# Kernel optimization log

Measured on AMD Instinct MI355X. Metric: run time of the kernel, lower is better.

The kernel has to match this reference:

```python
import jax, jax.numpy as jnp
import numpy as np

BS, N, T, D, R = 64, 256, 32, 512, 8
DK = D // R  # 64 == key_feature_dim


def setup_inputs() -> dict:
    key = jax.random.key(0)
    ks = jax.random.split(key, 20)
    s = 0.02
    p = lambda k, shape: jax.random.normal(k, shape, jnp.float32) * s
    return {
        "v": jax.random.normal(ks[0], (BS, N, D), jnp.float32),
        "b": jax.random.normal(ks[1], (BS, N, D), jnp.float32),
        "v_mask": jnp.ones((BS, N), jnp.float32),
        "t": jax.random.normal(ks[2], (BS, T, D), jnp.float32),
        "t_mask": jnp.ones((BS, T), jnp.float32),
        "WG1_w": p(ks[3], (D, D)), "WG1_b": p(ks[4], (D,)),
        "WG2_w": p(ks[5], (D, D)), "WG2_b": p(ks[6], (D,)),
        "WK_w": p(ks[7], (D, D)), "WK_b": p(ks[8], (D,)),
        "WQ_w": p(ks[9], (D, D)), "WQ_b": p(ks[10], (D,)),
        "WV_w": p(ks[11], (D, D)), "WV_b": p(ks[12], (D,)),
        "tc_w": p(ks[13], (D, 1)), "tc_b": p(ks[14], (1,)),
        "tmap_w": p(ks[15], (D, N * N)), "tmap_b": p(ks[16], (N * N,)),
    }


def _forward(v, b, v_mask, t, t_mask,
             WG1_w, WG1_b, WG2_w, WG2_b, WK_w, WK_b, WQ_w, WQ_b, WV_w, WV_b,
             tc_w, tc_b, tmap_w, tmap_b):
    bs, num_obj, dim = v.shape
    n_rel = R
    dk = dim // n_rel  # dim_per_rel == dim_k

    def shape4(x):  # (bs, N, D) -> (bs, R, N, dk)
        return x.reshape(bs, num_obj, n_rel, dk).transpose(0, 2, 1, 3)

    # --- text summary branch ---
    t_m = t * t_mask[:, :, None]                       # (bs, T, D)
    tc = t_m @ tc_w + tc_b                             # (bs, T, 1)
    tc = jnp.where(t_mask[:, :, None] == 0, -jnp.inf, tc)
    t_sscore = jax.nn.sigmoid(tc)                      # sigmoid(-inf) = 0 for pad
    t_summary = jnp.einsum('btd,bt->bd', t_m, t_sscore[..., 0])   # (bs, D)
    tmap = jax.nn.relu(t_summary @ tmap_w + tmap_b)
    tmap = tmap.reshape(bs, 1, num_obj, num_obj)       # broadcast over relations

    # --- geometric pairwise score ---
    wg1 = shape4((b @ WG1_w + WG1_b) * v_mask[:, :, None])
    wg2 = shape4((b @ WG2_w + WG2_b) * v_mask[:, :, None])
    w_g = jax.nn.relu(jnp.einsum('brnd,brmd->brnm', wg1, wg2)) + tmap

    # --- scaled dot-product score ---
    wk = shape4(v @ WK_w + WK_b)
    wq = shape4(v @ WQ_w + WQ_b)
    scaled_dot = jnp.einsum('brnd,brmd->brnm', wk, wq) / jnp.sqrt(jnp.float32(dk))

    # --- combine, mask, softmax, weighted sum ---
    w_mn = jnp.log(jnp.maximum(w_g, 1e-6)) + scaled_dot
    w_mn = jnp.where((v_mask == 0)[:, None, None, :], -jnp.inf, w_mn)
    attn = jax.nn.softmax(w_mn, axis=-1)               # (bs, R, N, N)

    wv = shape4(v @ WV_w + WV_b)
    out = jnp.einsum('brnm,brmd->brnd', attn, wv)
    out = out.transpose(0, 2, 1, 3).reshape(bs, num_obj, dim)
    return out + v


def reference(v, b, v_mask, t, t_mask,
              WG1_w, WG1_b, WG2_w, WG2_b, WK_w, WK_b, WQ_w, WQ_b, WV_w, WV_b,
              tc_w, tc_b, tmap_w, tmap_b):
    return _forward(v, b, v_mask, t, t_mask,
                    WG1_w, WG1_b, WG2_w, WG2_b, WK_w, WK_b, WQ_w, WQ_b,
                    WV_w, WV_b, tc_w, tc_b, tmap_w, tmap_b)
```

## Files before the change

kernel.cpp:

```cpp
#include <hip/hip_runtime.h>
#include <math.h>

#define BS 64
#define NOBJ 256
#define TTOK 32
#define DIM 512
#define NREL 8
#define DKK 64
#define NN 65536

typedef __attribute__((ext_vector_type(8))) short bf16x8;
typedef __attribute__((ext_vector_type(4))) float f32x4;

__device__ __forceinline__ unsigned short f2bf(float x) {
    union { float f; unsigned int u; } c; c.f = x;
    unsigned int u = c.u;
    return (unsigned short)((u + 0x7fffu + ((u >> 16) & 1u)) >> 16);
}
__device__ __forceinline__ float bf2f(unsigned short h) {
    union { unsigned int u; float f; } c; c.u = ((unsigned int)h) << 16;
    return c.f;
}
__device__ __forceinline__ void gl2lds16(const unsigned short* g, unsigned short* l) {
    __builtin_amdgcn_global_load_lds((const __attribute__((address_space(1))) void*)g,
                                     (__attribute__((address_space(3))) void*)l, 16, 0, 0);
}

__global__ void k_text(const float* __restrict__ tt, const float* __restrict__ t_mask,
                       const float* __restrict__ tc_w, const float* __restrict__ tc_b,
                       unsigned short* __restrict__ ts_bf) {
    int b = blockIdx.x;
    int tid = threadIdx.x;
    __shared__ float red[TTOK][8];
    __shared__ float sc[TTOK];
    {
        int tok = tid >> 3, seg = tid & 7;
        const float* tp = tt + (size_t)(b * TTOK + tok) * DIM + seg * 64;
        const float* wp = tc_w + seg * 64;
        float s = 0.f;
#pragma unroll
        for (int i = 0; i < 16; ++i) {
            float4 a = *(const float4*)(tp + i * 4);
            float4 w = *(const float4*)(wp + i * 4);
            s += a.x * w.x + a.y * w.y + a.z * w.z + a.w * w.w;
        }
        red[tok][seg] = s;
    }
    __syncthreads();
    if (tid < TTOK) {
        float s = 0.f;
#pragma unroll
        for (int i = 0; i < 8; ++i) s += red[tid][i];
        float m = t_mask[b * TTOK + tid];
        float tc = m * s + tc_b[0];
        float sig = 1.f / (1.f + __expf(-tc));
        sc[tid] = (m != 0.f) ? m * sig : 0.f;
    }
    __syncthreads();
    for (int d = tid; d < DIM; d += 256) {
        float acc = 0.f;
#pragma unroll
        for (int tok = 0; tok < TTOK; ++tok)
            acc += tt[(size_t)(b * TTOK + tok) * DIM + d] * sc[tok];
        ts_bf[b * DIM + d] = f2bf(acc);
    }
}

__global__ void k_convert(const float* __restrict__ v, const float* __restrict__ b,
                          unsigned short* __restrict__ v_bf, unsigned short* __restrict__ b_bf) {
    const float* src = blockIdx.y ? b : v;
    unsigned short* dst = blockIdx.y ? b_bf : v_bf;
    size_t i = ((size_t)blockIdx.x * 256 + threadIdx.x) * 4;
    float4 a = *(const float4*)(src + i);
    ushort4 o;
    o.x = f2bf(a.x); o.y = f2bf(a.y); o.z = f2bf(a.z); o.w = f2bf(a.w);
    *(ushort4*)(dst + i) = o;
}

__global__ void k_wt(const float* __restrict__ w0, const float* __restrict__ w1,
                     const float* __restrict__ w2, const float* __restrict__ w3,
                     const float* __restrict__ w4, unsigned short* __restrict__ WT) {
    int wsel = blockIdx.z;
    const float* W = wsel == 0 ? w0 : wsel == 1 ? w1 : wsel == 2 ? w2 : wsel == 3 ? w3 : w4;
    int k0 = blockIdx.x * 64, d0 = blockIdx.y * 64;
    __shared__ float tile[64][65];
    int tid = threadIdx.x;
#pragma unroll
    for (int p = 0; p < 16; ++p) {
        int lin = p * 256 + tid;
        int kk = lin >> 6, dd = lin & 63;
        tile[kk][dd] = W[(size_t)(k0 + kk) * DIM + d0 + dd];
    }
    __syncthreads();
    unsigned short* outp = WT + (size_t)wsel * DIM * DIM;
#pragma unroll
    for (int p = 0; p < 16; ++p) {
        int lin = p * 256 + tid;
        int dd = lin >> 6, kk = lin & 63;
        outp[(size_t)(d0 + dd) * DIM + k0 + kk] = f2bf(tile[kk][dd]);
    }
}

__launch_bounds__(256)
__global__ void k_tmap(const unsigned short* __restrict__ ts_bf,
                       const float* __restrict__ tmap_w, const float* __restrict__ tmap_b,
                       unsigned short* __restrict__ tmap) {
    int j0 = blockIdx.x * 64;
    int tid = threadIdx.x;
    int w = tid >> 6, lane = tid & 63, q = lane >> 4, li = lane & 15;
    __shared__ __align__(16) unsigned short Bt[64][40];
    f32x4 acc[4];
#pragma unroll
    for (int ct = 0; ct < 4; ++ct) acc[ct] = (f32x4){0.f, 0.f, 0.f, 0.f};

    for (int ks = 0; ks < 16; ++ks) {
        int k0 = ks * 32;
#pragma unroll
        for (int p = 0; p < 8; ++p) {
            int kk = (tid >> 6) + p * 4;
            int c = tid & 63;
            Bt[c][kk] = f2bf(tmap_w[(size_t)(k0 + kk) * NN + j0 + c]);
        }
        __syncthreads();
        bf16x8 a = *(const bf16x8*)(ts_bf + (size_t)(w * 16 + li) * DIM + k0 + q * 8);
#pragma unroll
        for (int ct = 0; ct < 4; ++ct) {
            bf16x8 bb = *(const bf16x8*)(&Bt[ct * 16 + li][q * 8]);
            acc[ct] = __builtin_amdgcn_mfma_f32_16x16x32_bf16(a, bb, acc[ct], 0, 0, 0);
        }
        __syncthreads();
    }
#pragma unroll
    for (int ct = 0; ct < 4; ++ct) {
        int j = j0 + ct * 16 + li;
        float bias = tmap_b[j];
#pragma unroll
        for (int i = 0; i < 4; ++i) {
            int bb = w * 16 + q * 4 + i;
            float val = fmaxf(acc[ct][i] + bias, 0.f);
            tmap[(size_t)bb * NN + j] = f2bf(val);
        }
    }
}

__launch_bounds__(256)
__global__ void k_proj(const unsigned short* __restrict__ v_bf, const unsigned short* __restrict__ b_bf,
                       const unsigned short* __restrict__ WT,
                       const float* __restrict__ bias0, const float* __restrict__ bias1,
                       const float* __restrict__ bias2, const float* __restrict__ bias3,
                       const float* __restrict__ bias4, const float* __restrict__ v_mask,
                       unsigned short* __restrict__ wg1, unsigned short* __restrict__ wg2,
                       unsigned short* __restrict__ wk, unsigned short* __restrict__ wq,
                       unsigned short* __restrict__ wvT) {
    int bx = blockIdx.x;
    int by = blockIdx.y;
    int m0 = bx * 128;
    int wsel = by >> 2;
    const unsigned short* A = (wsel < 2) ? b_bf : v_bf;
    int tid = threadIdx.x;
    int w = tid >> 6, lane = tid & 63, q = lane >> 4, li = lane & 15;
    int rh = w & 1, ch = w >> 1;

    __shared__ __align__(16) unsigned short smem[128 * 136];
    unsigned short* As = smem;
    unsigned short* Bs = smem + 4096;

    f32x4 acc[4][4];
#pragma unroll
    for (int rt = 0; rt < 4; ++rt)
#pragma unroll
        for (int ct = 0; ct < 4; ++ct) acc[rt][ct] = (f32x4){0.f, 0.f, 0.f, 0.f};

    const unsigned short* WTb = WT + (size_t)by * 128 * DIM;

    int rho = lane >> 2;
    int qs = (lane & 3) ^ ((lane >> 3) & 3);
    int rA0 = w * 16 + rho, rA1 = (w + 4) * 16 + rho;
    const unsigned short* Ag0 = A + (size_t)(m0 + rA0) * DIM + qs * 8;
    const unsigned short* Ag1 = A + (size_t)(m0 + rA1) * DIM + qs * 8;
    const unsigned short* Bg0 = WTb + (size_t)rA0 * DIM + qs * 8;
    const unsigned short* Bg1 = WTb + (size_t)rA1 * DIM + qs * 8;
    unsigned short* Al0 = As + w * 512;
    unsigned short* Al1 = As + (w + 4) * 512;
    unsigned short* Bl0 = Bs + w * 512;
    unsigned short* Bl1 = Bs + (w + 4) * 512;

    int sseg = (q ^ ((li >> 1) & 3)) * 8;

    for (int ks = 0; ks < 16; ++ks) {
        int k0 = ks * 32;
        gl2lds16(Ag0 + k0, Al0);
        gl2lds16(Ag1 + k0, Al1);
        gl2lds16(Bg0 + k0, Bl0);
        gl2lds16(Bg1 + k0, Bl1);
        __syncthreads();
        bf16x8 af[4], bfr[4];
#pragma unroll
        for (int rt = 0; rt < 4; ++rt)
            af[rt] = *(const bf16x8*)(As + (rh * 64 + rt * 16 + li) * 32 + sseg);
#pragma unroll
        for (int ct = 0; ct < 4; ++ct)
            bfr[ct] = *(const bf16x8*)(Bs + (ch * 64 + ct * 16 + li) * 32 + sseg);
#pragma unroll
        for (int rt = 0; rt < 4; ++rt)
#pragma unroll
            for (int ct = 0; ct < 4; ++ct)
                acc[rt][ct] = __builtin_amdgcn_mfma_f32_16x16x32_bf16(af[rt], bfr[ct], acc[rt][ct], 0, 0, 0);
        __syncthreads();
    }

    const float* bias = wsel == 0 ? bias0 : wsel == 1 ? bias1 : wsel == 2 ? bias2 : wsel == 3 ? bias3 : bias4;
    int dblk = (by & 3) * 128;

    if (wsel < 4) {
#pragma unroll
        for (int ct = 0; ct < 4; ++ct) {
            int d = dblk + ch * 64 + ct * 16 + li;
            float bs = bias[d];
#pragma unroll
            for (int rt = 0; rt < 4; ++rt) {
#pragma unroll
                for (int i = 0; i < 4; ++i) {
                    int bn = m0 + rh * 64 + rt * 16 + q * 4 + i;
                    float val = acc[rt][ct][i] + bs;
                    if (wsel < 2) val *= v_mask[bn];
                    unsigned short h = f2bf(val);
                    if (wsel == 0)      wg1[(size_t)bn * DIM + d] = h;
                    else if (wsel == 1) wg2[(size_t)bn * DIM + d] = h;
                    else if (wsel == 2) wk[(size_t)bn * DIM + d] = h;
                    else                wq[(size_t)bn * DIM + d] = h;
                }
            }
        }
    } else {
        unsigned short (*T)[136] = (unsigned short (*)[136])smem;
#pragma unroll
        for (int ct = 0; ct < 4; ++ct) {
            int d_local = ch * 64 + ct * 16 + li;
            float bs = bias[dblk + d_local];
#pragma unroll
            for (int rt = 0; rt < 4; ++rt) {
#pragma unroll
                for (int i = 0; i < 4; ++i) {
                    int n_local = rh * 64 + rt * 16 + q * 4 + i;
                    T[d_local][n_local] = f2bf(acc[rt][ct][i] + bs);
                }
            }
        }
        __syncthreads();
        int b = m0 >> 8, nbase = m0 & 255;
        int dl = tid >> 1;
        int nh = (tid & 1) * 64;
        int d = dblk + dl;
        int rr = d >> 6, dk = d & 63;
        unsigned short* dst = wvT + ((size_t)(b * NREL + rr) * DKK + dk) * NOBJ + nbase + nh;
#pragma unroll
        for (int k = 0; k < 8; ++k)
            *(bf16x8*)(dst + k * 8) = *(const bf16x8*)(&T[dl][nh + k * 8]);
    }
}

__launch_bounds__(256)
__global__ void k_attn(const unsigned short* __restrict__ wg1, const unsigned short* __restrict__ wg2,
                       const unsigned short* __restrict__ wk, const unsigned short* __restrict__ wq,
                       const unsigned short* __restrict__ wvT,
                       const unsigned short* __restrict__ tmap, const float* __restrict__ v_mask,
                       const float* __restrict__ v, float* __restrict__ out) {
    int br = blockIdx.x;
    int nt = blockIdx.y;
    int b = br >> 3, r = br & 7;
    int n0 = nt * 32;
    int tid = threadIdx.x;
    int w = tid >> 6, lane = tid & 63, q = lane >> 4, li = lane & 15;
    int rt = w & 1, ch = w >> 1;

    __shared__ __align__(16) unsigned short P_lds[32][264];
    __shared__ float redmax[2][32];
    __shared__ float redsum[2][32];
    __shared__ float linv[32];

    bf16x8 ag[2], ak[2];
    {
        int n = n0 + rt * 16 + li;
        const unsigned short* g1p = wg1 + (size_t)(b * NOBJ + n) * DIM + r * DKK;
        const unsigned short* kp  = wk  + (size_t)(b * NOBJ + n) * DIM + r * DKK;
#pragma unroll
        for (int ks = 0; ks < 2; ++ks) {
            ag[ks] = *(const bf16x8*)(g1p + ks * 32 + q * 8);
            ak[ks] = *(const bf16x8*)(kp + ks * 32 + q * 8);
        }
    }

    float sreg[32];
    float mloc[4] = {-INFINITY, -INFINITY, -INFINITY, -INFINITY};
#pragma unroll
    for (int j8 = 0; j8 < 8; ++j8) {
        int j = ch * 8 + j8;
        int mcol = j * 16 + li;
        const unsigned short* g2p = wg2 + (size_t)(b * NOBJ + mcol) * DIM + r * DKK;
        const unsigned short* qp  = wq  + (size_t)(b * NOBJ + mcol) * DIM + r * DKK;
        f32x4 accG = (f32x4){0.f, 0.f, 0.f, 0.f};
        f32x4 accK = (f32x4){0.f, 0.f, 0.f, 0.f};
#pragma unroll
        for (int ks = 0; ks < 2; ++ks) {
            bf16x8 bg = *(const bf16x8*)(g2p + ks * 32 + q * 8);
            accG = __builtin_amdgcn_mfma_f32_16x16x32_bf16(ag[ks], bg, accG, 0, 0, 0);
            bf16x8 bq = *(const bf16x8*)(qp + ks * 32 + q * 8);
            accK = __builtin_amdgcn_mfma_f32_16x16x32_bf16(ak[ks], bq, accK, 0, 0, 0);
        }
        float vm = v_mask[b * NOBJ + mcol];
#pragma unroll
        for (int i = 0; i < 4; ++i) {
            int n = n0 + rt * 16 + q * 4 + i;
            float tm = bf2f(tmap[(size_t)b * NN + n * 256 + mcol]);
            float g = fmaxf(accG[i], 0.f) + tm;
            float s = __logf(fmaxf(g, 1e-6f)) + accK[i] * 0.125f;
            if (vm == 0.f) s = -INFINITY;
            sreg[j8 * 4 + i] = s;
            mloc[i] = fmaxf(mloc[i], s);
        }
    }
#pragma unroll
    for (int i = 0; i < 4; ++i) {
        float m = mloc[i];
        m = fmaxf(m, __shfl_xor(m, 1));
        m = fmaxf(m, __shfl_xor(m, 2));
        m = fmaxf(m, __shfl_xor(m, 4));
        m = fmaxf(m, __shfl_xor(m, 8));
        mloc[i] = m;
    }
    if (li == 0) {
#pragma unroll
        for (int i = 0; i < 4; ++i) redmax[ch][rt * 16 + q * 4 + i] = mloc[i];
    }
    __syncthreads();
    float rowM[4], sloc[4];
#pragma unroll
    for (int i = 0; i < 4; ++i) {
        int row = rt * 16 + q * 4 + i;
        rowM[i] = fmaxf(redmax[0][row], redmax[1][row]);
        sloc[i] = 0.f;
    }
#pragma unroll
    for (int j8 = 0; j8 < 8; ++j8) {
        int j = ch * 8 + j8;
#pragma unroll
        for (int i = 0; i < 4; ++i) {
            float p = __expf(sreg[j8 * 4 + i] - rowM[i]);
            sloc[i] += p;
            P_lds[rt * 16 + q * 4 + i][j * 16 + li] = f2bf(p);
        }
    }
#pragma unroll
    for (int i = 0; i < 4; ++i) {
        float s = sloc[i];
        s += __shfl_xor(s, 1);
        s += __shfl_xor(s, 2);
        s += __shfl_xor(s, 4);
        s += __shfl_xor(s, 8);
        sloc[i] = s;
    }
    if (li == 0) {
#pragma unroll
        for (int i = 0; i < 4; ++i) redsum[ch][rt * 16 + q * 4 + i] = sloc[i];
    }
    __syncthreads();
    if (tid < 32) linv[tid] = 1.f / (redsum[0][tid] + redsum[1][tid]);
    __syncthreads();

    f32x4 o[2];
    o[0] = (f32x4){0.f, 0.f, 0.f, 0.f};
    o[1] = (f32x4){0.f, 0.f, 0.f, 0.f};
#pragma unroll
    for (int ks = 0; ks < 8; ++ks) {
        bf16x8 a = *(const bf16x8*)(&P_lds[rt * 16 + li][ks * 32 + q * 8]);
#pragma unroll
        for (int c2 = 0; c2 < 2; ++c2) {
            int dkc = (ch * 2 + c2) * 16 + li;
            bf16x8 bb = *(const bf16x8*)(wvT + (size_t)(br * DKK + dkc) * NOBJ + ks * 32 + q * 8);
            o[c2] = __builtin_amdgcn_mfma_f32_16x16x32_bf16(a, bb, o[c2], 0, 0, 0);
        }
    }
#pragma unroll
    for (int c2 = 0; c2 < 2; ++c2) {
        int dkc = (ch * 2 + c2) * 16 + li;
        int d = r * DKK + dkc;
#pragma unroll
        for (int i = 0; i < 4; ++i) {
            int row = rt * 16 + q * 4 + i;
            int n = n0 + row;
            size_t idx = (size_t)(b * NOBJ + n) * DIM + d;
            out[idx] = o[c2][i] * linv[row] + v[idx];
        }
    }
}

extern "C" void kernel_launch(void* const* d_in, const int* in_sizes, int n_in,
                              void* d_out, int out_size, void* d_ws, size_t ws_size,
                              hipStream_t stream) {
    const float* v      = (const float*)d_in[0];
    const float* b      = (const float*)d_in[1];
    const float* v_mask = (const float*)d_in[2];
    const float* t      = (const float*)d_in[3];
    const float* t_mask = (const float*)d_in[4];
    const float* WG1_w  = (const float*)d_in[5];
    const float* WG1_b  = (const float*)d_in[6];
    const float* WG2_w  = (const float*)d_in[7];
    const float* WG2_b  = (const float*)d_in[8];
    const float* WK_w   = (const float*)d_in[9];
    const float* WK_b   = (const float*)d_in[10];
    const float* WQ_w   = (const float*)d_in[11];
    const float* WQ_b   = (const float*)d_in[12];
    const float* WV_w   = (const float*)d_in[13];
    const float* WV_b   = (const float*)d_in[14];
    const float* tc_w   = (const float*)d_in[15];
    const float* tc_b   = (const float*)d_in[16];
    const float* tmap_w = (const float*)d_in[17];
    const float* tmap_b = (const float*)d_in[18];
    float* out = (float*)d_out;

    char* ws = (char*)d_ws;
    size_t off = 0;
    auto alloc = [&](size_t bytes) {
        void* p = ws + off;
        off += (bytes + 255) & ~(size_t)255;
        return p;
    };
    unsigned short* ts_bf = (unsigned short*)alloc((size_t)BS * DIM * 2);
    unsigned short* tmap  = (unsigned short*)alloc((size_t)BS * NN * 2);
    unsigned short* v_bf  = (unsigned short*)alloc((size_t)BS * NOBJ * DIM * 2);
    unsigned short* b_bf  = (unsigned short*)alloc((size_t)BS * NOBJ * DIM * 2);
    unsigned short* WT    = (unsigned short*)alloc((size_t)5 * DIM * DIM * 2);
    unsigned short* wg1   = (unsigned short*)alloc((size_t)BS * NOBJ * DIM * 2);
    unsigned short* wg2   = (unsigned short*)alloc((size_t)BS * NOBJ * DIM * 2);
    unsigned short* wk    = (unsigned short*)alloc((size_t)BS * NOBJ * DIM * 2);
    unsigned short* wq    = (unsigned short*)alloc((size_t)BS * NOBJ * DIM * 2);
    unsigned short* wvT   = (unsigned short*)alloc((size_t)BS * NOBJ * DIM * 2);

    k_text<<<dim3(BS), dim3(256), 0, stream>>>(t, t_mask, tc_w, tc_b, ts_bf);
    k_convert<<<dim3(8192, 2), dim3(256), 0, stream>>>(v, b, v_bf, b_bf);
    k_wt<<<dim3(8, 8, 5), dim3(256), 0, stream>>>(WG1_w, WG2_w, WK_w, WQ_w, WV_w, WT);
    k_tmap<<<dim3(1024), dim3(256), 0, stream>>>(ts_bf, tmap_w, tmap_b, tmap);
    k_proj<<<dim3(128, 20), dim3(256), 0, stream>>>(v_bf, b_bf, WT,
                                                    WG1_b, WG2_b, WK_b, WQ_b, WV_b, v_mask,
                                                    wg1, wg2, wk, wq, wvT);
    k_attn<<<dim3(512, 8), dim3(256), 0, stream>>>(wg1, wg2, wk, wq, wvT, tmap, v_mask, v, out);
}
```

Measured before the change: 499.8 us.

## Restructure attention into per-wave online softmax and single-wave tmap GEMM

The attention kernel now runs one block per (batch, relation). Each wave owns 64 query rows and streams key columns in chunks of 32 with an online-softmax (flash-style) accumulator, so the cross-wave LDS reductions and block barriers go away. The tmap GEMM is rewritten as a 64-thread block that loads the weights straight from global into registers and reuses each B fragment across four row tiles, with no LDS staging or syncs. The trade-off is much higher register pressure (large accumulator arrays) and only 512 attention blocks, which could hurt occupancy. The tmap kernel also does strided scalar global loads of the weights.

```diff
diff --git a/kernel.cpp b/kernel.cpp
--- a/kernel.cpp
+++ b/kernel.cpp
@@ -101,44 +101,49 @@
     }
 }
 
-__launch_bounds__(256)
+__launch_bounds__(64)
 __global__ void k_tmap(const unsigned short* __restrict__ ts_bf,
                        const float* __restrict__ tmap_w, const float* __restrict__ tmap_b,
                        unsigned short* __restrict__ tmap) {
-    int j0 = blockIdx.x * 64;
-    int tid = threadIdx.x;
-    int w = tid >> 6, lane = tid & 63, q = lane >> 4, li = lane & 15;
-    __shared__ __align__(16) unsigned short Bt[64][40];
-    f32x4 acc[4];
-#pragma unroll
-    for (int ct = 0; ct < 4; ++ct) acc[ct] = (f32x4){0.f, 0.f, 0.f, 0.f};
-
-    for (int ks = 0; ks < 16; ++ks) {
-        int k0 = ks * 32;
-#pragma unroll
-        for (int p = 0; p < 8; ++p) {
-            int kk = (tid >> 6) + p * 4;
-            int c = tid & 63;
-            Bt[c][kk] = f2bf(tmap_w[(size_t)(k0 + kk) * NN + j0 + c]);
-        }
-        __syncthreads();
-        bf16x8 a = *(const bf16x8*)(ts_bf + (size_t)(w * 16 + li) * DIM + k0 + q * 8);
+    int col0 = blockIdx.x * 64;
+    int lane = threadIdx.x;
+    int q = lane >> 4, li = lane & 15;
+    f32x4 acc[4][4];
+#pragma unroll
+    for (int rt = 0; rt < 4; ++rt)
+#pragma unroll
+        for (int ct = 0; ct < 4; ++ct) acc[rt][ct] = (f32x4){0.f, 0.f, 0.f, 0.f};
+
+    for (int kt = 0; kt < 16; ++kt) {
+        int k0 = kt * 32;
+        bf16x8 a[4];
+#pragma unroll
+        for (int rt = 0; rt < 4; ++rt)
+            a[rt] = *(const bf16x8*)(ts_bf + (size_t)(rt * 16 + li) * DIM + k0 + q * 8);
 #pragma unroll
         for (int ct = 0; ct < 4; ++ct) {
-            bf16x8 bb = *(const bf16x8*)(&Bt[ct * 16 + li][q * 8]);
-            acc[ct] = __builtin_amdgcn_mfma_f32_16x16x32_bf16(a, bb, acc[ct], 0, 0, 0);
-        }
-        __syncthreads();
+            const float* wp = tmap_w + (size_t)(k0 + q * 8) * NN + col0 + ct * 16 + li;
+            bf16x8 bb;
+#pragma unroll
+            for (int j = 0; j < 8; ++j)
+                bb[j] = (short)f2bf(wp[(size_t)j * NN]);
+#pragma unroll
+            for (int rt = 0; rt < 4; ++rt)
+                acc[rt][ct] = __builtin_amdgcn_mfma_f32_16x16x32_bf16(a[rt], bb, acc[rt][ct], 0, 0, 0);
+        }
     }
 #pragma unroll
     for (int ct = 0; ct < 4; ++ct) {
-        int j = j0 + ct * 16 + li;
+        int j = col0 + ct * 16 + li;
         float bias = tmap_b[j];
 #pragma unroll
-        for (int i = 0; i < 4; ++i) {
-            int bb = w * 16 + q * 4 + i;
-            float val = fmaxf(acc[ct][i] + bias, 0.f);
-            tmap[(size_t)bb * NN + j] = f2bf(val);
+        for (int rt = 0; rt < 4; ++rt) {
+#pragma unroll
+            for (int i = 0; i < 4; ++i) {
+                int bb = rt * 16 + q * 4 + i;
+                float val = fmaxf(acc[rt][ct][i] + bias, 0.f);
+                tmap[(size_t)bb * NN + j] = f2bf(val);
+            }
         }
     }
 }
@@ -267,130 +272,137 @@
                        const unsigned short* __restrict__ tmap, const float* __restrict__ v_mask,
                        const float* __restrict__ v, float* __restrict__ out) {
     int br = blockIdx.x;
-    int nt = blockIdx.y;
     int b = br >> 3, r = br & 7;
-    int n0 = nt * 32;
     int tid = threadIdx.x;
     int w = tid >> 6, lane = tid & 63, q = lane >> 4, li = lane & 15;
-    int rt = w & 1, ch = w >> 1;
-
-    __shared__ __align__(16) unsigned short P_lds[32][264];
-    __shared__ float redmax[2][32];
-    __shared__ float redsum[2][32];
-    __shared__ float linv[32];
-
-    bf16x8 ag[2], ak[2];
+
+    __shared__ __align__(16) unsigned short P_lds[4][64][36];
+
+    bf16x8 ag[4][2], ak[4][2];
     {
-        int n = n0 + rt * 16 + li;
-        const unsigned short* g1p = wg1 + (size_t)(b * NOBJ + n) * DIM + r * DKK;
-        const unsigned short* kp  = wk  + (size_t)(b * NOBJ + n) * DIM + r * DKK;
-#pragma unroll
-        for (int ks = 0; ks < 2; ++ks) {
-            ag[ks] = *(const bf16x8*)(g1p + ks * 32 + q * 8);
-            ak[ks] = *(const bf16x8*)(kp + ks * 32 + q * 8);
-        }
-    }
-
-    float sreg[32];
-    float mloc[4] = {-INFINITY, -INFINITY, -INFINITY, -INFINITY};
-#pragma unroll
-    for (int j8 = 0; j8 < 8; ++j8) {
-        int j = ch * 8 + j8;
-        int mcol = j * 16 + li;
-        const unsigned short* g2p = wg2 + (size_t)(b * NOBJ + mcol) * DIM + r * DKK;
-        const unsigned short* qp  = wq  + (size_t)(b * NOBJ + mcol) * DIM + r * DKK;
-        f32x4 accG = (f32x4){0.f, 0.f, 0.f, 0.f};
-        f32x4 accK = (f32x4){0.f, 0.f, 0.f, 0.f};
-#pragma unroll
-        for (int ks = 0; ks < 2; ++ks) {
-            bf16x8 bg = *(const bf16x8*)(g2p + ks * 32 + q * 8);
-            accG = __builtin_amdgcn_mfma_f32_16x16x32_bf16(ag[ks], bg, accG, 0, 0, 0);
-            bf16x8 bq = *(const bf16x8*)(qp + ks * 32 + q * 8);
-            accK = __builtin_amdgcn_mfma_f32_16x16x32_bf16(ak[ks], bq, accK, 0, 0, 0);
-        }
-        float vm = v_mask[b * NOBJ + mcol];
-#pragma unroll
-        for (int i = 0; i < 4; ++i) {
-            int n = n0 + rt * 16 + q * 4 + i;
-            float tm = bf2f(tmap[(size_t)b * NN + n * 256 + mcol]);
-            float g = fmaxf(accG[i], 0.f) + tm;
-            float s = __logf(fmaxf(g, 1e-6f)) + accK[i] * 0.125f;
-            if (vm == 0.f) s = -INFINITY;
-            sreg[j8 * 4 + i] = s;
-            mloc[i] = fmaxf(mloc[i], s);
-        }
-    }
-#pragma unroll
-    for (int i = 0; i < 4; ++i) {
-        float m = mloc[i];
-        m = fmaxf(m, __shfl_xor(m, 1));
-        m = fmaxf(m, __shfl_xor(m, 2));
-        m = fmaxf(m, __shfl_xor(m, 4));
-        m = fmaxf(m, __shfl_xor(m, 8));
-        mloc[i] = m;
-    }
-    if (li == 0) {
-#pragma unroll
-        for (int i = 0; i < 4; ++i) redmax[ch][rt * 16 + q * 4 + i] = mloc[i];
-    }
-    __syncthreads();
-    float rowM[4], sloc[4];
-#pragma unroll
-    for (int i = 0; i < 4; ++i) {
-        int row = rt * 16 + q * 4 + i;
-        rowM[i] = fmaxf(redmax[0][row], redmax[1][row]);
-        sloc[i] = 0.f;
-    }
-#pragma unroll
-    for (int j8 = 0; j8 < 8; ++j8) {
-        int j = ch * 8 + j8;
-#pragma unroll
-        for (int i = 0; i < 4; ++i) {
-            float p = __expf(sreg[j8 * 4 + i] - rowM[i]);
-            sloc[i] += p;
-            P_lds[rt * 16 + q * 4 + i][j * 16 + li] = f2bf(p);
-        }
-    }
-#pragma unroll
-    for (int i = 0; i < 4; ++i) {
-        float s = sloc[i];
-        s += __shfl_xor(s, 1);
-        s += __shfl_xor(s, 2);
-        s += __shfl_xor(s, 4);
-        s += __shfl_xor(s, 8);
-        sloc[i] = s;
-    }
-    if (li == 0) {
-#pragma unroll
-        for (int i = 0; i < 4; ++i) redsum[ch][rt * 16 + q * 4 + i] = sloc[i];
-    }
-    __syncthreads();
-    if (tid < 32) linv[tid] = 1.f / (redsum[0][tid] + redsum[1][tid]);
-    __syncthreads();
-
-    f32x4 o[2];
-    o[0] = (f32x4){0.f, 0.f, 0.f, 0.f};
-    o[1] = (f32x4){0.f, 0.f, 0.f, 0.f};
-#pragma unroll
-    for (int ks = 0; ks < 8; ++ks) {
-        bf16x8 a = *(const bf16x8*)(&P_lds[rt * 16 + li][ks * 32 + q * 8]);
-#pragma unroll
-        for (int c2 = 0; c2 < 2; ++c2) {
-            int dkc = (ch * 2 + c2) * 16 + li;
-            bf16x8 bb = *(const bf16x8*)(wvT + (size_t)(br * DKK + dkc) * NOBJ + ks * 32 + q * 8);
-            o[c2] = __builtin_amdgcn_mfma_f32_16x16x32_bf16(a, bb, o[c2], 0, 0, 0);
-        }
-    }
-#pragma unroll
-    for (int c2 = 0; c2 < 2; ++c2) {
-        int dkc = (ch * 2 + c2) * 16 + li;
-        int d = r * DKK + dkc;
-#pragma unroll
-        for (int i = 0; i < 4; ++i) {
-            int row = rt * 16 + q * 4 + i;
-            int n = n0 + row;
-            size_t idx = (size_t)(b * NOBJ + n) * DIM + d;
-            out[idx] = o[c2][i] * linv[row] + v[idx];
+        const unsigned short* g1b = wg1 + (size_t)(b * NOBJ + w * 64 + li) * DIM + r * DKK + q * 8;
+        const unsigned short* kb  = wk  + (size_t)(b * NOBJ + w * 64 + li) * DIM + r * DKK + q * 8;
+#pragma unroll
+        for (int rt = 0; rt < 4; ++rt)
+#pragma unroll
+            for (int kt = 0; kt < 2; ++kt) {
+                ag[rt][kt] = *(const bf16x8*)(g1b + (size_t)rt * 16 * DIM + kt * 32);
+                ak[rt][kt] = *(const bf16x8*)(kb + (size_t)rt * 16 * DIM + kt * 32);
+            }
+    }
+
+    f32x4 O[4][4];
+    float m_[4][4], l_[4][4];
+#pragma unroll
+    for (int rt = 0; rt < 4; ++rt) {
+#pragma unroll
+        for (int dt = 0; dt < 4; ++dt) O[rt][dt] = (f32x4){0.f, 0.f, 0.f, 0.f};
+#pragma unroll
+        for (int i = 0; i < 4; ++i) { m_[rt][i] = -INFINITY; l_[rt][i] = 0.f; }
+    }
+
+    const unsigned short* tb = tmap + ((size_t)b << 16) + (w * 64 + q * 4) * 256 + li;
+
+    for (int j = 0; j < 8; ++j) {
+        int c0 = j * 32;
+        bf16x8 bg[2][2], bq[2][2];
+        {
+            const unsigned short* g2b = wg2 + (size_t)(b * NOBJ + c0 + li) * DIM + r * DKK + q * 8;
+            const unsigned short* qb  = wq  + (size_t)(b * NOBJ + c0 + li) * DIM + r * DKK + q * 8;
+#pragma unroll
+            for (int ct = 0; ct < 2; ++ct)
+#pragma unroll
+                for (int kt = 0; kt < 2; ++kt) {
+                    bg[ct][kt] = *(const bf16x8*)(g2b + (size_t)ct * 16 * DIM + kt * 32);
+                    bq[ct][kt] = *(const bf16x8*)(qb + (size_t)ct * 16 * DIM + kt * 32);
+                }
+        }
+        float vm0 = v_mask[b * NOBJ + c0 + li];
+        float vm1 = v_mask[b * NOBJ + c0 + 16 + li];
+
+        float s[4][2][4];
+#pragma unroll
+        for (int rt = 0; rt < 4; ++rt) {
+#pragma unroll
+            for (int ct = 0; ct < 2; ++ct) {
+                f32x4 aG = (f32x4){0.f, 0.f, 0.f, 0.f};
+                f32x4 aK = (f32x4){0.f, 0.f, 0.f, 0.f};
+#pragma unroll
+                for (int kt = 0; kt < 2; ++kt) {
+                    aG = __builtin_amdgcn_mfma_f32_16x16x32_bf16(ag[rt][kt], bg[ct][kt], aG, 0, 0, 0);
+                    aK = __builtin_amdgcn_mfma_f32_16x16x32_bf16(ak[rt][kt], bq[ct][kt], aK, 0, 0, 0);
+                }
+                float vm = ct ? vm1 : vm0;
+#pragma unroll
+                for (int i = 0; i < 4; ++i) {
+                    float tm = bf2f(tb[(rt * 16 + i) * 256 + c0 + ct * 16]);
+                    float g = fmaxf(aG[i], 0.f) + tm;
+                    float sv = __logf(fmaxf(g, 1e-6f)) + aK[i] * 0.125f;
+                    s[rt][ct][i] = (vm == 0.f) ? -INFINITY : sv;
+                }
+            }
+        }
+#pragma unroll
+        for (int rt = 0; rt < 4; ++rt) {
+            float alpha[4];
+#pragma unroll
+            for (int i = 0; i < 4; ++i) {
+                float tmax = fmaxf(s[rt][0][i], s[rt][1][i]);
+                tmax = fmaxf(tmax, __shfl_xor(tmax, 1));
+                tmax = fmaxf(tmax, __shfl_xor(tmax, 2));
+                tmax = fmaxf(tmax, __shfl_xor(tmax, 4));
+                tmax = fmaxf(tmax, __shfl_xor(tmax, 8));
+                float mo = m_[rt][i];
+                float mn = fmaxf(mo, tmax);
+                float al = (mo == -INFINITY) ? 0.f : __expf(mo - mn);
+                m_[rt][i] = mn;
+                alpha[i] = al;
+                float p0 = __expf(s[rt][0][i] - mn);
+                float p1 = __expf(s[rt][1][i] - mn);
+                float ps = p0 + p1;
+                ps += __shfl_xor(ps, 1);
+                ps += __shfl_xor(ps, 2);
+                ps += __shfl_xor(ps, 4);
+                ps += __shfl_xor(ps, 8);
+                l_[rt][i] = l_[rt][i] * al + ps;
+                int row = rt * 16 + q * 4 + i;
+                P_lds[w][row][li] = f2bf(p0);
+                P_lds[w][row][16 + li] = f2bf(p1);
+            }
+#pragma unroll
+            for (int dt = 0; dt < 4; ++dt) {
+                f32x4 o = O[rt][dt];
+                o[0] *= alpha[0]; o[1] *= alpha[1]; o[2] *= alpha[2]; o[3] *= alpha[3];
+                O[rt][dt] = o;
+            }
+        }
+        bf16x8 pa[4], vb[4];
+#pragma unroll
+        for (int rt = 0; rt < 4; ++rt)
+            pa[rt] = *(const bf16x8*)(&P_lds[w][rt * 16 + li][q * 8]);
+#pragma unroll
+        for (int dt = 0; dt < 4; ++dt)
+            vb[dt] = *(const bf16x8*)(wvT + (size_t)(br * DKK + dt * 16 + li) * NOBJ + c0 + q * 8);
+#pragma unroll
+        for (int rt = 0; rt < 4; ++rt)
+#pragma unroll
+            for (int dt = 0; dt < 4; ++dt)
+                O[rt][dt] = __builtin_amdgcn_mfma_f32_16x16x32_bf16(pa[rt], vb[dt], O[rt][dt], 0, 0, 0);
+    }
+
+#pragma unroll
+    for (int rt = 0; rt < 4; ++rt) {
+        float linv[4];
+#pragma unroll
+        for (int i = 0; i < 4; ++i) linv[i] = 1.f / l_[rt][i];
+#pragma unroll
+        for (int dt = 0; dt < 4; ++dt) {
+#pragma unroll
+            for (int i = 0; i < 4; ++i) {
+                int n = w * 64 + rt * 16 + q * 4 + i;
+                size_t idx = (size_t)(b * NOBJ + n) * DIM + r * DKK + dt * 16 + li;
+                out[idx] = O[rt][dt][i] * linv[i] + v[idx];
+            }
         }
     }
 }
@@ -440,9 +452,9 @@
     k_text<<<dim3(BS), dim3(256), 0, stream>>>(t, t_mask, tc_w, tc_b, ts_bf);
     k_convert<<<dim3(8192, 2), dim3(256), 0, stream>>>(v, b, v_bf, b_bf);
     k_wt<<<dim3(8, 8, 5), dim3(256), 0, stream>>>(WG1_w, WG2_w, WK_w, WQ_w, WV_w, WT);
-    k_tmap<<<dim3(1024), dim3(256), 0, stream>>>(ts_bf, tmap_w, tmap_b, tmap);
+    k_tmap<<<dim3(1024), dim3(64), 0, stream>>>(ts_bf, tmap_w, tmap_b, tmap);
     k_proj<<<dim3(128, 20), dim3(256), 0, stream>>>(v_bf, b_bf, WT,
                                                     WG1_b, WG2_b, WK_b, WQ_b, WV_b, v_mask,
                                                     wg1, wg2, wk, wq, wvT);
-    k_attn<<<dim3(512, 8), dim3(256), 0, stream>>>(wg1, wg2, wk, wq, wvT, tmap, v_mask, v, out);
-}
+    k_attn<<<dim3(512), dim3(256), 0, stream>>>(wg1, wg2, wk, wq, wvT, tmap, v_mask, v, out);
+}
```

After: 494.4 us. Within noise of the previous version (-1.1%).
